# Kernel optimization log

Hardware: AMD Instinct MI355X
Metric: run time of the kernel (lower is better)

Reference implementation:

```python
import jax, jax.numpy as jnp
import numpy as np

_DN = ('NCHW', 'OIHW', 'NCHW')


def setup_inputs() -> dict:
    key = jax.random.key(0)
    k1, k2 = jax.random.split(key)
    x = jax.random.normal(k1, (32, 3, 224, 224), dtype=jnp.float32)
    memes = jax.random.normal(k2, (64, 3, 7, 7), dtype=jnp.float32)
    return {"x": x, "memes": memes}


def reference(x, memes):
    # x: [B, C, H, W], memes: [K, C, kh, kw]
    # x_m = cross-correlation of x with templates -> [B, K, H', W']
    x_m = jax.lax.conv_general_dilated(x, memes, window_strides=(1, 1),
                                       padding='VALID', dimension_numbers=_DN)
    # x2 = conv2d(x**2, ones_like(memes)): every output channel is identical
    # (all-ones kernel), so compute once with a single-channel ones kernel and
    # let broadcasting replicate it across the K template channels.
    ones_k = jnp.ones((1,) + memes.shape[1:], dtype=x.dtype)  # [1, C, kh, kw]
    x2 = jax.lax.conv_general_dilated(x * x, ones_k, window_strides=(1, 1),
                                      padding='VALID', dimension_numbers=_DN)  # [B,1,H',W']
    # m2 = sum(weight**2 over (2,3), keepdim).sum(dim=1) -> [K, 1, 1]
    m2 = jnp.sum(memes * memes, axis=(1, 2, 3)).reshape(-1, 1, 1)
    # Normalized squared Euclidean distance between each patch and template.
    return (x2 - 2.0 * x_m + m2) / m2
```

## Files before the change

### kernel.cpp

```cpp
#include <hip/hip_runtime.h>

#define NB 32
#define NC 3
#define NK 64
#define KS 7
#define IH 224
#define IW 224
#define OH 218
#define OW 218
#define OHW (OH * OW)
#define ROWS 8

typedef float  f32x4  __attribute__((ext_vector_type(4)));
typedef float  f32x16 __attribute__((ext_vector_type(16)));
typedef short  s16x8  __attribute__((ext_vector_type(8)));
typedef unsigned long long u64;

static __device__ __forceinline__ unsigned short f2bf(float f) {
  unsigned int u = __float_as_uint(f);
  u += 0x7FFFu + ((u >> 16) & 1u);
  return (unsigned short)(u >> 16);
}

static __device__ __forceinline__ int swz(int r, int ci) {
  return (((ci >> 3) ^ ((r >> 1) & 3)) << 3) | (ci & 7);
}


__global__ void k_prep_xrow(const float* __restrict__ x, unsigned short* __restrict__ xb,
                            float* __restrict__ t) {
  __shared__ float s_lds[IW];
  const int n  = blockIdx.x;
  const int b  = n / IH;
  const int h  = n - b * IH;
  const int px = threadIdx.x;
  if (px < IW) {
    float acc = 0.f;
#pragma unroll
    for (int c = 0; c < NC; ++c) {
      size_t idx = ((size_t)(b * NC + c) * IH + h) * IW + px;
      float v = x[idx];
      xb[idx] = f2bf(v);
      acc += v * v;
    }
    s_lds[px] = acc;
  }
  __syncthreads();
  if (px < OW) {
    float acc = 0.f;
#pragma unroll
    for (int j = 0; j < KS; ++j) acc += s_lds[px + j];
    t[(size_t)(b * IH + h) * OW + px] = acc;
  }
}

__global__ void k_colbox(const float* __restrict__ t, float* __restrict__ x2) {
  int n = blockIdx.x * 256 + threadIdx.x;
  if (n >= NB * OH * OW) return;
  int b = n / (OH * OW);
  int r = n - b * (OH * OW);
  int oh = r / OW;
  int ow = r - oh * OW;
  const float* col = t + (size_t)(b * IH + oh) * OW + ow;
  float acc = 0.f;
#pragma unroll
  for (int i = 0; i < KS; ++i) acc += col[i * OW];
  x2[n] = acc;
}

__global__ void k_prep_w(const float* __restrict__ memes, unsigned short* __restrict__ WTg,
                         float* __restrict__ m2inv) {
  __shared__ float red[3];
  const int k = blockIdx.x, t = threadIdx.x;
  float v = 0.f;
  if (t < 147) v = memes[k * 147 + t];
  float s = v * v;
#pragma unroll
  for (int sh = 32; sh > 0; sh >>= 1) s += __shfl_down(s, sh, 64);
  if ((t & 63) == 0) red[t >> 6] = s;
  __syncthreads();
  if (t == 0) m2inv[k] = 1.0f / (red[0] + red[1] + red[2]);
  if (t < 147) {
    int c = t / 49, rem = t - 49 * c, i = rem / 7, j = rem - 7 * i;
    int row = j * NK + k;
    WTg[row * 32 + swz(row, c * 7 + i)] = f2bf(v);
  }
  for (int idx = t; idx < 7 * 11; idx += 192) {
    int j = idx / 11, ci = 21 + (idx - 11 * j);
    int row = j * NK + k;
    WTg[row * 32 + swz(row, ci)] = 0;
  }
}

static __device__ __forceinline__ void xt_issue(u64 v[2],
    const unsigned short* __restrict__ xb, int b, int oh, int ow0, int tid) {
#pragma unroll
  for (int m = 0; m < 2; ++m) {
    int idx = tid + 256 * m;
    u64 val = 0;
    if (idx < 378) {
      int tq = idx % 18;
      int ci = idx / 18;
      int c  = ci / 7;
      int i  = ci - 7 * c;
      val = *(const u64*)&xb[((size_t)(b * NC + c) * IH + oh + i) * IW + ow0 + 4 * tq];
    }
    v[m] = val;
  }
}

static __device__ __forceinline__ void xt_write(unsigned short* __restrict__ XT,
    const u64 v[2], int tid) {
#pragma unroll
  for (int m = 0; m < 2; ++m) {
    int idx = tid + 256 * m;
    if (idx < 378) {
      int tq = idx % 18;
      int ci = idx / 18;
#pragma unroll
      for (int e = 0; e < 4; ++e) {
        int t = 4 * tq + e;
        XT[t * 32 + swz(t, ci)] = (unsigned short)(v[m] >> (16 * e));
      }
    }
  }
}

__global__ __launch_bounds__(256, 4) void k_main(
    const unsigned short* __restrict__ xb, const float* __restrict__ x2g,
    const unsigned short* __restrict__ WTg, const float* __restrict__ m2inv,
    float* __restrict__ out, float* __restrict__ dump) {
  __shared__ __align__(16) unsigned short WTl[KS * NK * 32];
  __shared__ __align__(16) unsigned short XTl[2][72 * 32];

  const int tid  = threadIdx.x;
  const int w    = tid >> 6;
  const int lane = tid & 63;
  const int l31  = lane & 31;
  const int hsel = lane >> 5;
  const int kh   = w >> 1;
  const int ph   = w & 1;

  const int wg = blockIdx.x;
  const int sw = (wg & 7) * 448 + (wg >> 3);
  const int ow0 = (sw & 3) * 64;
  const int ohb = ((sw >> 2) % 28) * ROWS;
  const int b   = sw / 112;

  for (int ch = w; ch < 28; ch += 4) {
    const unsigned short* g = WTg + ch * 512 + lane * 8;
    unsigned short* l = WTl + ch * 512;
    __builtin_amdgcn_global_load_lds((const __attribute__((address_space(1))) void*)g,
                                     (__attribute__((address_space(3))) void*)l, 16, 0, 0);
  }

  f32x4 m2r[4];
  {
    const float* mp = m2inv + kh * 32 + 4 * hsel;
#pragma unroll
    for (int g = 0; g < 4; ++g) m2r[g] = *(const f32x4*)&mp[8 * g];
  }

  for (int idx = tid; idx < 2 * 72; idx += 256) {
    int bb = idx / 72, t = idx - 72 * bb;
    unsigned short* row = &XTl[bb][t * 32];
    const int m = (t >> 1) & 3;
    *(uint4*)&row[(3 ^ m) << 3] = (uint4){0, 0, 0, 0};
    const int b2 = (2 ^ m) << 3;
    row[b2 + 5] = 0; row[b2 + 6] = 0; row[b2 + 7] = 0;
  }

  u64 s0[2];
  xt_issue(s0, xb, b, ohb, ow0, tid);
  xt_write(&XTl[0][0], s0, tid);
  asm volatile("s_waitcnt vmcnt(0) lgkmcnt(0)" ::: "memory");
  __builtin_amdgcn_s_barrier();

  const int swzA = (l31 >> 1) & 3;
  const int tB   = ph * 32 + l31;
  const int ow   = ow0 + tB;

#pragma unroll 1
  for (int r = 0; r < ROWS; ++r) {
    const int oh = ohb + r;
    const bool more = (r + 1 < ROWS);

    u64 sn[2];
    if (more) xt_issue(sn, xb, b, oh + 1, ow0, tid);

    const bool ok = (ow < OW) && (oh < OH);
    const float x2v = x2g[(size_t)(b * OH + (ok ? oh : 0)) * OW + (ok ? ow : 0)];

    const unsigned short* XT = &XTl[r & 1][0];
    f32x16 accA = {0.f,0.f,0.f,0.f,0.f,0.f,0.f,0.f,0.f,0.f,0.f,0.f,0.f,0.f,0.f,0.f};
    f32x16 accB = accA;

#pragma unroll
    for (int j = 0; j < KS; ++j) {
      const unsigned short* ar = WTl + (j * 64 + kh * 32 + l31) * 32;
      s16x8 aA = *(const s16x8*)&ar[(hsel ^ swzA) << 3];
      s16x8 aB = *(const s16x8*)&ar[((2 + hsel) ^ swzA) << 3];
      const int t = tB + j;
      const unsigned short* br = XT + t * 32;
      const int swzB = (t >> 1) & 3;
      s16x8 bA = *(const s16x8*)&br[(hsel ^ swzB) << 3];
      s16x8 bB = *(const s16x8*)&br[((2 + hsel) ^ swzB) << 3];
      accA = __builtin_amdgcn_mfma_f32_32x32x16_bf16(aA, bA, accA, 0, 0, 0);
      accB = __builtin_amdgcn_mfma_f32_32x32x16_bf16(aB, bB, accB, 0, 0, 0);
    }
    const f32x16 acc = accA + accB;

    float* ob = ok ? out + ((size_t)(b * NK + kh * 32) * OH + oh) * OW + ow : dump + tid;
    const size_t ks = ok ? (size_t)OHW : 0;
#pragma unroll
    for (int reg = 0; reg < 16; ++reg) {
      const int kk = (reg & 3) + 8 * (reg >> 2) + 4 * hsel;
      ob[(size_t)kk * ks] = (x2v - 2.0f * acc[reg]) * m2r[reg >> 2][reg & 3] + 1.0f;
    }

    if (more) {
      xt_write(&XTl[(r + 1) & 1][0], sn, tid);
      asm volatile("s_waitcnt lgkmcnt(0)" ::: "memory");
      __builtin_amdgcn_s_barrier();
    }
  }
}

extern "C" void kernel_launch(void* const* d_in, const int* in_sizes, int n_in,
                              void* d_out, int out_size, void* d_ws, size_t ws_size,
                              hipStream_t stream) {
  const float* x     = (const float*)d_in[0];
  const float* memes = (const float*)d_in[1];
  float* out = (float*)d_out;

  char* ws = (char*)d_ws;
  unsigned short* xb  = (unsigned short*)(ws);
  float* t            = (float*)(ws + 9633792);
  float* x2           = (float*)(ws + 15884288);
  unsigned short* WTg = (unsigned short*)(ws + 21967360);
  float* m2inv        = (float*)(ws + 21996032);
  float* dump         = (float*)(ws + 21996544);

  (void)in_sizes; (void)n_in; (void)out_size; (void)ws_size;

  k_prep_xrow<<<NB * IH, 256, 0, stream>>>(x, xb, t);
  k_colbox<<<(NB * OH * OW + 255) / 256, 256, 0, stream>>>(t, x2);
  k_prep_w<<<NK, 192, 0, stream>>>(memes, WTg, m2inv);

  k_main<<<4 * 28 * NB, 256, 0, stream>>>(xb, x2, WTg, m2inv, out, dump);
}
```

Measured before the change: 159.2 us.

## Keep weight fragments in registers and stage output through LDS for coalesced stores

Weight MFMA fragments are loaded once per block from global memory into registers, removing the swizzled LDS weight buffer and its per-iteration LDS reads. Accumulators are written to an LDS tile and read back row-wise, so each k-channel's output row is stored as contiguous vector writes with explicit edge masking. This replaces the scattered per-lane strided stores and the dummy dump buffer. It costs an extra barrier and LDS round trip per output row, plus more vector registers for the weight fragments.

```diff
diff --git a/kernel.cpp b/kernel.cpp
--- a/kernel.cpp
+++ b/kernel.cpp
@@ -11,6 +11,7 @@
 #define OHW (OH * OW)
 #define ROWS 8
 
+typedef float  f32x2  __attribute__((ext_vector_type(2)));
 typedef float  f32x4  __attribute__((ext_vector_type(4)));
 typedef float  f32x16 __attribute__((ext_vector_type(16)));
 typedef short  s16x8  __attribute__((ext_vector_type(8)));
@@ -82,13 +83,11 @@
   if (t == 0) m2inv[k] = 1.0f / (red[0] + red[1] + red[2]);
   if (t < 147) {
     int c = t / 49, rem = t - 49 * c, i = rem / 7, j = rem - 7 * i;
-    int row = j * NK + k;
-    WTg[row * 32 + swz(row, c * 7 + i)] = f2bf(v);
+    WTg[(j * NK + k) * 32 + (c * 7 + i)] = f2bf(v);
   }
   for (int idx = t; idx < 7 * 11; idx += 192) {
     int j = idx / 11, ci = 21 + (idx - 11 * j);
-    int row = j * NK + k;
-    WTg[row * 32 + swz(row, ci)] = 0;
+    WTg[(j * NK + k) * 32 + ci] = 0;
   }
 }
 
@@ -129,37 +128,35 @@
 __global__ __launch_bounds__(256, 4) void k_main(
     const unsigned short* __restrict__ xb, const float* __restrict__ x2g,
     const unsigned short* __restrict__ WTg, const float* __restrict__ m2inv,
-    float* __restrict__ out, float* __restrict__ dump) {
-  __shared__ __align__(16) unsigned short WTl[KS * NK * 32];
+    float* __restrict__ out) {
   __shared__ __align__(16) unsigned short XTl[2][72 * 32];
+  __shared__ __align__(16) float OT[NK][64];
+  __shared__ float m2l[NK];
 
   const int tid  = threadIdx.x;
+  const int lane = tid & 63;
   const int w    = tid >> 6;
-  const int lane = tid & 63;
   const int l31  = lane & 31;
   const int hsel = lane >> 5;
   const int kh   = w >> 1;
   const int ph   = w & 1;
 
-  const int wg = blockIdx.x;
-  const int sw = (wg & 7) * 448 + (wg >> 3);
+  const int wg  = blockIdx.x;
+  const int sw  = (wg & 7) * 448 + (wg >> 3);
   const int ow0 = (sw & 3) * 64;
   const int ohb = ((sw >> 2) % 28) * ROWS;
   const int b   = sw / 112;
 
-  for (int ch = w; ch < 28; ch += 4) {
-    const unsigned short* g = WTg + ch * 512 + lane * 8;
-    unsigned short* l = WTl + ch * 512;
-    __builtin_amdgcn_global_load_lds((const __attribute__((address_space(1))) void*)g,
-                                     (__attribute__((address_space(3))) void*)l, 16, 0, 0);
-  }
-
-  f32x4 m2r[4];
+  s16x8 Af[KS][2];
   {
-    const float* mp = m2inv + kh * 32 + 4 * hsel;
-#pragma unroll
-    for (int g = 0; g < 4; ++g) m2r[g] = *(const f32x4*)&mp[8 * g];
-  }
+    const unsigned short* ap = WTg + ((size_t)(kh * 32 + l31) * 32 + hsel * 8);
+#pragma unroll
+    for (int j = 0; j < KS; ++j) {
+      Af[j][0] = *(const s16x8*)&ap[j * (NK * 32)];
+      Af[j][1] = *(const s16x8*)&ap[j * (NK * 32) + 16];
+    }
+  }
+  if (tid < NK) m2l[tid] = m2inv[tid];
 
   for (int idx = tid; idx < 2 * 72; idx += 256) {
     int bb = idx / 72, t = idx - 72 * bb;
@@ -173,12 +170,15 @@
   u64 s0[2];
   xt_issue(s0, xb, b, ohb, ow0, tid);
   xt_write(&XTl[0][0], s0, tid);
-  asm volatile("s_waitcnt vmcnt(0) lgkmcnt(0)" ::: "memory");
+  asm volatile("s_waitcnt lgkmcnt(0)" ::: "memory");
   __builtin_amdgcn_s_barrier();
 
-  const int swzA = (l31 >> 1) & 3;
   const int tB   = ph * 32 + l31;
-  const int ow   = ow0 + tB;
+  const int g16  = tid >> 4;
+  const int l16  = tid & 15;
+  const bool edge = (ow0 + 64 > OW);
+  const float* x2b = x2g + (size_t)b * OH * OW + ow0 + l16 * 4;
+  float* outb = out + (size_t)b * NK * OHW + ow0 + l16 * 4;
 
 #pragma unroll 1
   for (int r = 0; r < ROWS; ++r) {
@@ -188,34 +188,54 @@
     u64 sn[2];
     if (more) xt_issue(sn, xb, b, oh + 1, ow0, tid);
 
-    const bool ok = (ow < OW) && (oh < OH);
-    const float x2v = x2g[(size_t)(b * OH + (ok ? oh : 0)) * OW + (ok ? ow : 0)];
-
     const unsigned short* XT = &XTl[r & 1][0];
     f32x16 accA = {0.f,0.f,0.f,0.f,0.f,0.f,0.f,0.f,0.f,0.f,0.f,0.f,0.f,0.f,0.f,0.f};
     f32x16 accB = accA;
 
 #pragma unroll
     for (int j = 0; j < KS; ++j) {
-      const unsigned short* ar = WTl + (j * 64 + kh * 32 + l31) * 32;
-      s16x8 aA = *(const s16x8*)&ar[(hsel ^ swzA) << 3];
-      s16x8 aB = *(const s16x8*)&ar[((2 + hsel) ^ swzA) << 3];
       const int t = tB + j;
       const unsigned short* br = XT + t * 32;
       const int swzB = (t >> 1) & 3;
       s16x8 bA = *(const s16x8*)&br[(hsel ^ swzB) << 3];
       s16x8 bB = *(const s16x8*)&br[((2 + hsel) ^ swzB) << 3];
-      accA = __builtin_amdgcn_mfma_f32_32x32x16_bf16(aA, bA, accA, 0, 0, 0);
-      accB = __builtin_amdgcn_mfma_f32_32x32x16_bf16(aB, bB, accB, 0, 0, 0);
+      accA = __builtin_amdgcn_mfma_f32_32x32x16_bf16(Af[j][0], bA, accA, 0, 0, 0);
+      accB = __builtin_amdgcn_mfma_f32_32x32x16_bf16(Af[j][1], bB, accB, 0, 0, 0);
     }
     const f32x16 acc = accA + accB;
 
-    float* ob = ok ? out + ((size_t)(b * NK + kh * 32) * OH + oh) * OW + ow : dump + tid;
-    const size_t ks = ok ? (size_t)OHW : 0;
-#pragma unroll
-    for (int reg = 0; reg < 16; ++reg) {
-      const int kk = (reg & 3) + 8 * (reg >> 2) + 4 * hsel;
-      ob[(size_t)kk * ks] = (x2v - 2.0f * acc[reg]) * m2r[reg >> 2][reg & 3] + 1.0f;
+    if (oh < OH) {
+#pragma unroll
+      for (int reg = 0; reg < 16; ++reg)
+        OT[kh * 32 + 4 * hsel + 8 * (reg >> 2) + (reg & 3)][tB] = acc[reg];
+      asm volatile("s_waitcnt lgkmcnt(0)" ::: "memory");
+      __builtin_amdgcn_s_barrier();
+
+      const float* x2p = x2b + (size_t)oh * OW;
+      f32x2 x2lo = *(const f32x2*)&x2p[0];
+      f32x2 x2hi = *(const f32x2*)&x2p[2];
+#pragma unroll
+      for (int i = 0; i < 4; ++i) {
+        const int k = g16 + 16 * i;
+        f32x4 v = *(const f32x4*)&OT[k][l16 * 4];
+        const float ms = m2l[k];
+        f32x2 rlo, rhi;
+        rlo[0] = (x2lo[0] - 2.0f * v[0]) * ms + 1.0f;
+        rlo[1] = (x2lo[1] - 2.0f * v[1]) * ms + 1.0f;
+        rhi[0] = (x2hi[0] - 2.0f * v[2]) * ms + 1.0f;
+        rhi[1] = (x2hi[1] - 2.0f * v[3]) * ms + 1.0f;
+        float* op = outb + (size_t)k * OHW + (size_t)oh * OW;
+        if (!edge) {
+          *(f32x2*)&op[0] = rlo;
+          *(f32x2*)&op[2] = rhi;
+        } else {
+          const int base = l16 * 4, lim = OW - ow0;
+          if (base     < lim) op[0] = rlo[0];
+          if (base + 1 < lim) op[1] = rlo[1];
+          if (base + 2 < lim) op[2] = rhi[0];
+          if (base + 3 < lim) op[3] = rhi[1];
+        }
+      }
     }
 
     if (more) {
@@ -237,9 +257,8 @@
   unsigned short* xb  = (unsigned short*)(ws);
   float* t            = (float*)(ws + 9633792);
   float* x2           = (float*)(ws + 15884288);
-  unsigned short* WTg = (unsigned short*)(ws + 21967360);
-  float* m2inv        = (float*)(ws + 21996032);
-  float* dump         = (float*)(ws + 21996544);
+  unsigned short* WTg = (unsigned short*)(ws + 21967872);
+  float* m2inv        = (float*)(ws + 21996544);
 
   (void)in_sizes; (void)n_in; (void)out_size; (void)ws_size;
 
@@ -247,5 +266,5 @@
   k_colbox<<<(NB * OH * OW + 255) / 256, 256, 0, stream>>>(t, x2);
   k_prep_w<<<NK, 192, 0, stream>>>(memes, WTg, m2inv);
 
-  k_main<<<4 * 28 * NB, 256, 0, stream>>>(xb, x2, WTg, m2inv, out, dump);
-}
+  k_main<<<4 * 28 * NB, 256, 0, stream>>>(xb, x2, WTg, m2inv, out);
+}
```

Measured after the change: 257.9 us. +62.0%, slower.

## Retile main conv kernel to full-width row panels with per-block kernel-half

Applied to the files above, without the earlier changes.

Each block now covers a full 218-wide output row panel of 7 rows for one half (32) of the templates, instead of a 64-wide column strip of 8 rows for all 64 templates. The input row slab is staged once per row for the full width, which removes the redundant 6-pixel halo loads between adjacent column strips, and each block loads only its half of the weights. The 7x7 weight layout is reordered so each half is contiguous. The XT buffer is now single-buffered with an extra barrier per row, which gives up some overlap of staging and compute. The lower wave has an uneven second tile, so work is imbalanced across waves.

```diff
diff --git a/kernel.cpp b/kernel.cpp
--- a/kernel.cpp
+++ b/kernel.cpp
@@ -9,7 +9,8 @@
 #define OH 218
 #define OW 218
 #define OHW (OH * OW)
-#define ROWS 8
+#define P 7
+#define SLOTS (21 * 58)
 
 typedef float  f32x4  __attribute__((ext_vector_type(4)));
 typedef float  f32x16 __attribute__((ext_vector_type(16)));
@@ -82,45 +83,45 @@
   if (t == 0) m2inv[k] = 1.0f / (red[0] + red[1] + red[2]);
   if (t < 147) {
     int c = t / 49, rem = t - 49 * c, i = rem / 7, j = rem - 7 * i;
-    int row = j * NK + k;
+    int row = (k >> 5) * 224 + j * 32 + (k & 31);
     WTg[row * 32 + swz(row, c * 7 + i)] = f2bf(v);
   }
   for (int idx = t; idx < 7 * 11; idx += 192) {
     int j = idx / 11, ci = 21 + (idx - 11 * j);
-    int row = j * NK + k;
+    int row = (k >> 5) * 224 + j * 32 + (k & 31);
     WTg[row * 32 + swz(row, ci)] = 0;
   }
 }
 
-static __device__ __forceinline__ void xt_issue(u64 v[2],
-    const unsigned short* __restrict__ xb, int b, int oh, int ow0, int tid) {
-#pragma unroll
-  for (int m = 0; m < 2; ++m) {
+static __device__ __forceinline__ void xt_issue(u64 v[5],
+    const unsigned short* __restrict__ xb, int b, int oh, int tid) {
+#pragma unroll
+  for (int m = 0; m < 5; ++m) {
     int idx = tid + 256 * m;
     u64 val = 0;
-    if (idx < 378) {
-      int tq = idx % 18;
-      int ci = idx / 18;
+    if (idx < SLOTS) {
+      int ci = idx / 58;
+      int q  = idx - 58 * ci;
       int c  = ci / 7;
       int i  = ci - 7 * c;
-      val = *(const u64*)&xb[((size_t)(b * NC + c) * IH + oh + i) * IW + ow0 + 4 * tq];
+      val = *(const u64*)&xb[((size_t)(b * NC + c) * IH + oh + i) * IW + 4 * q];
     }
     v[m] = val;
   }
 }
 
 static __device__ __forceinline__ void xt_write(unsigned short* __restrict__ XT,
-    const u64 v[2], int tid) {
-#pragma unroll
-  for (int m = 0; m < 2; ++m) {
+    const u64 v[5], int tid) {
+#pragma unroll
+  for (int m = 0; m < 5; ++m) {
     int idx = tid + 256 * m;
-    if (idx < 378) {
-      int tq = idx % 18;
-      int ci = idx / 18;
+    if (idx < SLOTS) {
+      int ci = idx / 58;
+      int q  = idx - 58 * ci;
 #pragma unroll
       for (int e = 0; e < 4; ++e) {
-        int t = 4 * tq + e;
-        XT[t * 32 + swz(t, ci)] = (unsigned short)(v[m] >> (16 * e));
+        int px = 4 * q + e;
+        XT[px * 32 + swz(px, ci)] = (unsigned short)(v[m] >> (16 * e));
       }
     }
   }
@@ -129,26 +130,26 @@
 __global__ __launch_bounds__(256, 4) void k_main(
     const unsigned short* __restrict__ xb, const float* __restrict__ x2g,
     const unsigned short* __restrict__ WTg, const float* __restrict__ m2inv,
-    float* __restrict__ out, float* __restrict__ dump) {
-  __shared__ __align__(16) unsigned short WTl[KS * NK * 32];
-  __shared__ __align__(16) unsigned short XTl[2][72 * 32];
+    float* __restrict__ out) {
+  __shared__ __align__(16) unsigned short WTl[KS * 32 * 32];
+  __shared__ __align__(16) unsigned short XTl[232 * 32];
 
   const int tid  = threadIdx.x;
   const int w    = tid >> 6;
   const int lane = tid & 63;
   const int l31  = lane & 31;
   const int hsel = lane >> 5;
-  const int kh   = w >> 1;
-  const int ph   = w & 1;
-
-  const int wg = blockIdx.x;
-  const int sw = (wg & 7) * 448 + (wg >> 3);
-  const int ow0 = (sw & 3) * 64;
-  const int ohb = ((sw >> 2) % 28) * ROWS;
-  const int b   = sw / 112;
-
-  for (int ch = w; ch < 28; ch += 4) {
-    const unsigned short* g = WTg + ch * 512 + lane * 8;
+
+  const int wg    = blockIdx.x;
+  const int sw    = (wg & 7) * 256 + (wg >> 3);
+  const int b     = sw >> 6;
+  const int rm    = sw & 63;
+  const int panel = rm >> 1;
+  const int kh    = rm & 1;
+  const int oh0   = panel * P;
+
+  for (int ch = w; ch < 14; ch += 4) {
+    const unsigned short* g = WTg + kh * 7168 + ch * 512 + lane * 8;
     unsigned short* l = WTl + ch * 512;
     __builtin_amdgcn_global_load_lds((const __attribute__((address_space(1))) void*)g,
                                      (__attribute__((address_space(3))) void*)l, 16, 0, 0);
@@ -161,65 +162,87 @@
     for (int g = 0; g < 4; ++g) m2r[g] = *(const f32x4*)&mp[8 * g];
   }
 
-  for (int idx = tid; idx < 2 * 72; idx += 256) {
-    int bb = idx / 72, t = idx - 72 * bb;
-    unsigned short* row = &XTl[bb][t * 32];
-    const int m = (t >> 1) & 3;
+  for (int px = tid; px < 232; px += 256) {
+    unsigned short* row = &XTl[px * 32];
+    const int m = (px >> 1) & 3;
     *(uint4*)&row[(3 ^ m) << 3] = (uint4){0, 0, 0, 0};
     const int b2 = (2 ^ m) << 3;
     row[b2 + 5] = 0; row[b2 + 6] = 0; row[b2 + 7] = 0;
   }
 
-  u64 s0[2];
-  xt_issue(s0, xb, b, ohb, ow0, tid);
-  xt_write(&XTl[0][0], s0, tid);
+  u64 s0[5];
+  xt_issue(s0, xb, b, oh0, tid);
+  xt_write(XTl, s0, tid);
   asm volatile("s_waitcnt vmcnt(0) lgkmcnt(0)" ::: "memory");
   __builtin_amdgcn_s_barrier();
 
   const int swzA = (l31 >> 1) & 3;
-  const int tB   = ph * 32 + l31;
-  const int ow   = ow0 + tB;
+  const int px0  = w * 32 + l31;
+  const int px1  = (w + 4) * 32 + l31;
+  const bool has1 = (w < 3);
 
 #pragma unroll 1
-  for (int r = 0; r < ROWS; ++r) {
-    const int oh = ohb + r;
-    const bool more = (r + 1 < ROWS);
-
-    u64 sn[2];
-    if (more) xt_issue(sn, xb, b, oh + 1, ow0, tid);
-
-    const bool ok = (ow < OW) && (oh < OH);
-    const float x2v = x2g[(size_t)(b * OH + (ok ? oh : 0)) * OW + (ok ? ow : 0)];
-
-    const unsigned short* XT = &XTl[r & 1][0];
-    f32x16 accA = {0.f,0.f,0.f,0.f,0.f,0.f,0.f,0.f,0.f,0.f,0.f,0.f,0.f,0.f,0.f,0.f};
-    f32x16 accB = accA;
+  for (int r = 0; r < P; ++r) {
+    const int oh = oh0 + r;
+    const bool more = (r + 1 < P);
+
+    u64 sn[5];
+    if (more) xt_issue(sn, xb, b, oh + 1, tid);
+
+    const bool okR = (oh < OH);
+    float x2v0 = 0.f, x2v1 = 0.f;
+    if (okR) x2v0 = x2g[(size_t)(b * OH + oh) * OW + px0];
+    if (okR && has1 && px1 < OW) x2v1 = x2g[(size_t)(b * OH + oh) * OW + px1];
+
+    f32x16 acc0 = {0.f,0.f,0.f,0.f,0.f,0.f,0.f,0.f,0.f,0.f,0.f,0.f,0.f,0.f,0.f,0.f};
+    f32x16 acc1 = acc0;
 
 #pragma unroll
     for (int j = 0; j < KS; ++j) {
-      const unsigned short* ar = WTl + (j * 64 + kh * 32 + l31) * 32;
+      const unsigned short* ar = WTl + (j * 32 + l31) * 32;
       s16x8 aA = *(const s16x8*)&ar[(hsel ^ swzA) << 3];
       s16x8 aB = *(const s16x8*)&ar[((2 + hsel) ^ swzA) << 3];
-      const int t = tB + j;
-      const unsigned short* br = XT + t * 32;
-      const int swzB = (t >> 1) & 3;
-      s16x8 bA = *(const s16x8*)&br[(hsel ^ swzB) << 3];
-      s16x8 bB = *(const s16x8*)&br[((2 + hsel) ^ swzB) << 3];
-      accA = __builtin_amdgcn_mfma_f32_32x32x16_bf16(aA, bA, accA, 0, 0, 0);
-      accB = __builtin_amdgcn_mfma_f32_32x32x16_bf16(aB, bB, accB, 0, 0, 0);
-    }
-    const f32x16 acc = accA + accB;
-
-    float* ob = ok ? out + ((size_t)(b * NK + kh * 32) * OH + oh) * OW + ow : dump + tid;
-    const size_t ks = ok ? (size_t)OHW : 0;
-#pragma unroll
-    for (int reg = 0; reg < 16; ++reg) {
-      const int kk = (reg & 3) + 8 * (reg >> 2) + 4 * hsel;
-      ob[(size_t)kk * ks] = (x2v - 2.0f * acc[reg]) * m2r[reg >> 2][reg & 3] + 1.0f;
-    }
-
+      {
+        const int t0 = px0 + j;
+        const unsigned short* br = XTl + t0 * 32;
+        const int sB = (t0 >> 1) & 3;
+        s16x8 bA = *(const s16x8*)&br[(hsel ^ sB) << 3];
+        s16x8 bB = *(const s16x8*)&br[((2 + hsel) ^ sB) << 3];
+        acc0 = __builtin_amdgcn_mfma_f32_32x32x16_bf16(aA, bA, acc0, 0, 0, 0);
+        acc0 = __builtin_amdgcn_mfma_f32_32x32x16_bf16(aB, bB, acc0, 0, 0, 0);
+      }
+      if (has1) {
+        const int t1 = px1 + j;
+        const unsigned short* br = XTl + t1 * 32;
+        const int sB = (t1 >> 1) & 3;
+        s16x8 bA = *(const s16x8*)&br[(hsel ^ sB) << 3];
+        s16x8 bB = *(const s16x8*)&br[((2 + hsel) ^ sB) << 3];
+        acc1 = __builtin_amdgcn_mfma_f32_32x32x16_bf16(aA, bA, acc1, 0, 0, 0);
+        acc1 = __builtin_amdgcn_mfma_f32_32x32x16_bf16(aB, bB, acc1, 0, 0, 0);
+      }
+    }
+
+    if (okR) {
+      float* ob0 = out + ((size_t)(b * NK + kh * 32) * OH + oh) * OW + px0;
+#pragma unroll
+      for (int reg = 0; reg < 16; ++reg) {
+        const int kk = (reg & 3) + 8 * (reg >> 2) + 4 * hsel;
+        ob0[(size_t)kk * OHW] = (x2v0 - 2.0f * acc0[reg]) * m2r[reg >> 2][reg & 3] + 1.0f;
+      }
+      if (has1 && px1 < OW) {
+        float* ob1 = out + ((size_t)(b * NK + kh * 32) * OH + oh) * OW + px1;
+#pragma unroll
+        for (int reg = 0; reg < 16; ++reg) {
+          const int kk = (reg & 3) + 8 * (reg >> 2) + 4 * hsel;
+          ob1[(size_t)kk * OHW] = (x2v1 - 2.0f * acc1[reg]) * m2r[reg >> 2][reg & 3] + 1.0f;
+        }
+      }
+    }
+
+    asm volatile("s_waitcnt lgkmcnt(0)" ::: "memory");
+    __builtin_amdgcn_s_barrier();
     if (more) {
-      xt_write(&XTl[(r + 1) & 1][0], sn, tid);
+      xt_write(XTl, sn, tid);
       asm volatile("s_waitcnt lgkmcnt(0)" ::: "memory");
       __builtin_amdgcn_s_barrier();
     }
@@ -239,7 +262,6 @@
   float* x2           = (float*)(ws + 15884288);
   unsigned short* WTg = (unsigned short*)(ws + 21967360);
   float* m2inv        = (float*)(ws + 21996032);
-  float* dump         = (float*)(ws + 21996544);
 
   (void)in_sizes; (void)n_in; (void)out_size; (void)ws_size;
 
@@ -247,5 +269,5 @@
   k_colbox<<<(NB * OH * OW + 255) / 256, 256, 0, stream>>>(t, x2);
   k_prep_w<<<NK, 192, 0, stream>>>(memes, WTg, m2inv);
 
-  k_main<<<4 * 28 * NB, 256, 0, stream>>>(xb, x2, WTg, m2inv, out, dump);
-}
+  k_main<<<2048, 256, 0, stream>>>(xb, x2, WTg, m2inv, out);
+}
```

Result: slower. 169.2 us (+6.3%).
